# Optimization experiments

Hardware: AMD Instinct MI355X
Metric: run time of the kernel (lower is better)

Reference implementation:

```python
import math
import jax, jax.numpy as jnp
import numpy as np

B, S, D, H, P, FF = 64, 100, 768, 8, 8, 3072
HD = D // H
NUM_LAYERS = 4
EPS = 1e-5


def _layernorm(x, g, b):
    m = jnp.mean(x, axis=-1, keepdims=True)
    v = jnp.mean(jnp.square(x - m), axis=-1, keepdims=True)
    return (x - m) * jax.lax.rsqrt(v + EPS) * g + b


def _positional_encoding(seq_len, d_model):
    pos = jnp.arange(seq_len, dtype=jnp.float32)[:, None]
    div = jnp.exp(jnp.arange(0, d_model, 2, dtype=jnp.float32) * (-math.log(10000.0) / d_model))
    pe = jnp.zeros((seq_len, d_model), dtype=jnp.float32)
    pe = pe.at[:, 0::2].set(jnp.sin(pos * div))
    pe = pe.at[:, 1::2].set(jnp.cos(pos * div))
    return pe[None]  # [1, S, D]


def setup_inputs() -> dict:
    key = jax.random.key(0)
    ks = jax.random.split(key, 12)
    s = 0.02
    return {
        "template_seq": jax.random.normal(ks[0], (B, S, D), jnp.float32),
        "param_seq": jax.random.normal(ks[1], (B, S, P, 768), jnp.float32),
        # ParamEncoder (shared across all 4 layers)
        "Wc": jax.random.normal(ks[2], (768, D), jnp.float32) * s,
        "bc": jnp.zeros((D,), jnp.float32),
        "gp": jnp.ones((D,), jnp.float32),
        "bp": jnp.zeros((D,), jnp.float32),
        # FFN (shared)
        "W1": jax.random.normal(ks[3], (D, FF), jnp.float32) * s,
        "b1": jnp.zeros((FF,), jnp.float32),
        "W2": jax.random.normal(ks[4], (FF, D), jnp.float32) * s,
        "b2": jnp.zeros((D,), jnp.float32),
        # LayerNorms (shared)
        "g1": jnp.ones((D,), jnp.float32),
        "bn1": jnp.zeros((D,), jnp.float32),
        "g2": jnp.ones((D,), jnp.float32),
        "bn2": jnp.zeros((D,), jnp.float32),
        # final classifier
        "Wfc": jax.random.normal(ks[5], (D * S, 2), jnp.float32) * s,
        "bfc": jnp.zeros((2,), jnp.float32),
    }


def _layer(src, param_seq, Wc, bc, gp, bp, W1, b1, W2, b2, g1, bn1, g2, bn2):
    inv_sqrt_hd = 1.0 / math.sqrt(HD)
    # ParamEncoder: Linear(768->D) per param vector, mean over params, LayerNorm.
    # Linear is linear => mean-then-project is identical to project-then-mean.
    pooled = jnp.mean(param_seq, axis=2)                  # [B, S, 768]
    param_enc = _layernorm(pooled @ Wc + bc, gp, bp)       # [B, S, D]
    pb = param_enc.reshape(B, S, H, HD).transpose(0, 2, 1, 3)  # [B, H, S, HD]
    param_bias = jnp.einsum('bhqd,bhkd->bhqk', pb, pb) * inv_sqrt_hd
    # attention with q = k = v = src (no projections in the original forward)
    q = src.reshape(B, S, H, HD).transpose(0, 2, 1, 3)     # [B, H, S, HD]
    attn = jnp.einsum('bhqd,bhkd->bhqk', q, q) * inv_sqrt_hd + param_bias
    attn = jax.nn.softmax(attn, axis=-1)
    out = jnp.einsum('bhqk,bhkd->bhqd', attn, q)
    out = out.transpose(0, 2, 1, 3).reshape(B, S, D)
    src = _layernorm(src + out, g1, bn1)
    ffn = jax.nn.gelu(src @ W1 + b1, approximate=False) @ W2 + b2
    return _layernorm(src + ffn, g2, bn2)


def reference(template_seq, param_seq, Wc, bc, gp, bp, W1, b1, W2, b2,
              g1, bn1, g2, bn2, Wfc, bfc):
    x = template_seq + _positional_encoding(S, D)
    for _ in range(NUM_LAYERS):
        x = _layer(x, param_seq, Wc, bc, gp, bp, W1, b1, W2, b2, g1, bn1, g2, bn2)
    return x.reshape(B, S * D) @ Wfc + bfc  # [B, 2]
```

## Files before the change

kernel.cpp:

```cpp
#include <hip/hip_runtime.h>
#include <hip/hip_bf16.h>
#include <math.h>


typedef __attribute__((ext_vector_type(8))) short bf16x8;
typedef __attribute__((ext_vector_type(4))) float f32x4;
typedef __attribute__((ext_vector_type(4))) short short4v;

#define BB 64
#define SS 100
#define DD 768
#define HH 8
#define HD 96
#define FF_ 3072
#define ROWS 6400
#define LN10000 9.210340371976184f

__device__ __forceinline__ void async_copy16(void* lds_dst, const void* gsrc) {
  __builtin_amdgcn_global_load_lds(
      (const __attribute__((address_space(1))) void*)gsrc,
      (__attribute__((address_space(3))) void*)lds_dst, 16, 0, 0);
}

__device__ __forceinline__ float block_sum256(float v, float* sbuf) {
#pragma unroll
  for (int o = 32; o > 0; o >>= 1) v += __shfl_xor(v, o, 64);
  int tid = threadIdx.x;
  __syncthreads();
  if ((tid & 63) == 0) sbuf[tid >> 6] = v;
  __syncthreads();
  return sbuf[0] + sbuf[1] + sbuf[2] + sbuf[3];
}

__device__ __forceinline__ float block_sum192(float v, float* sbuf) {
#pragma unroll
  for (int o = 32; o > 0; o >>= 1) v += __shfl_xor(v, o, 64);
  int tid = threadIdx.x;
  __syncthreads();
  if ((tid & 63) == 0) sbuf[tid >> 6] = v;
  __syncthreads();
  return sbuf[0] + sbuf[1] + sbuf[2];
}

__global__ void convert_transpose(const float* __restrict__ in,
                                  __hip_bfloat16* __restrict__ out,
                                  int K, int N) {
  __shared__ float t[32][33];
  int n0 = blockIdx.x * 32, k0 = blockIdx.y * 32;
  int tid = threadIdx.x;
  int tx = tid & 31, ty = tid >> 5;
#pragma unroll
  for (int j = 0; j < 32; j += 8)
    t[ty + j][tx] = in[(size_t)(k0 + ty + j) * N + n0 + tx];
  __syncthreads();
#pragma unroll
  for (int j = 0; j < 32; j += 8)
    out[(size_t)(n0 + ty + j) * K + k0 + tx] = __float2bfloat16(t[tx][ty + j]);
}

__global__ void pool_mean(const float* __restrict__ ps,
                          __hip_bfloat16* __restrict__ pooled) {
  int idx = blockIdx.x * 256 + threadIdx.x;
  int row = idx / DD, c = idx - row * DD;
  float s = 0.f;
#pragma unroll
  for (int p = 0; p < 8; p++) s += ps[(size_t)(row * 8 + p) * DD + c];
  pooled[idx] = __float2bfloat16(s * 0.125f);
}

__global__ void add_pe(const float* __restrict__ t, float* __restrict__ src) {
  int idx = blockIdx.x * 256 + threadIdx.x;
  int row = idx / DD, c = idx - row * DD;
  int srow = row % SS;
  int c2 = c & ~1;
  float ang = (float)srow * expf((float)c2 * (-LN10000 / (float)DD));
  float pe = (c & 1) ? cosf(ang) : sinf(ang);
  src[idx] = t[idx] + pe;
}

template <bool XB16, bool RESID, bool WB16>
__global__ void ln_row(const float* __restrict__ Xf,
                       const __hip_bfloat16* __restrict__ Xb,
                       const float* __restrict__ R,
                       const float* __restrict__ g, const float* __restrict__ bb,
                       float* __restrict__ of, __hip_bfloat16* __restrict__ ob) {
  int row = blockIdx.x, tid = threadIdx.x;
  size_t base = (size_t)row * DD;
  int c4 = tid * 4;
  float4 v;
  if constexpr (XB16) {
    short4v xv = *(const short4v*)(Xb + base + c4);
    __hip_bfloat16* p = (__hip_bfloat16*)&xv;
    v.x = __bfloat162float(p[0]); v.y = __bfloat162float(p[1]);
    v.z = __bfloat162float(p[2]); v.w = __bfloat162float(p[3]);
  } else {
    v = *(const float4*)(Xf + base + c4);
  }
  if (RESID) {
    float4 rv = *(const float4*)(R + base + c4);
    v.x += rv.x; v.y += rv.y; v.z += rv.z; v.w += rv.w;
  }
  __shared__ float sbuf[3];
  float s = block_sum192(v.x + v.y + v.z + v.w, sbuf);
  float mean = s * (1.0f / DD);
  float dx = v.x - mean, dy = v.y - mean, dz = v.z - mean, dw = v.w - mean;
  float ss = block_sum192(dx * dx + dy * dy + dz * dz + dw * dw, sbuf);
  float rs = rsqrtf(ss * (1.0f / DD) + 1e-5f);
  float4 gv = *(const float4*)(g + c4);
  float4 bv = *(const float4*)(bb + c4);
  float4 y;
  y.x = dx * rs * gv.x + bv.x;
  y.y = dy * rs * gv.y + bv.y;
  y.z = dz * rs * gv.z + bv.z;
  y.w = dw * rs * gv.w + bv.w;
  *(float4*)(of + base + c4) = y;
  if (WB16) {
    __hip_bfloat16 hb[4] = {__float2bfloat16(y.x), __float2bfloat16(y.y),
                            __float2bfloat16(y.z), __float2bfloat16(y.w)};
    *(short4v*)(ob + base + c4) = *(short4v*)hb;
  }
}

__launch_bounds__(256, 2)
__global__ void param_bias_mfma(const float* __restrict__ penc,
                                float* __restrict__ pbias) {
  __shared__ __align__(16) __hip_bfloat16 Qs[128][104];
  const int bh = blockIdx.x;
  const int b = bh >> 3, h = bh & 7;
  const int tid = threadIdx.x;
  const int wave = tid >> 6, lane = tid & 63;
  const int r = lane & 15, quad = lane >> 4;
  const int q8 = quad * 8;
  const int wr = (wave >> 1) * 64, wc = (wave & 1) * 64;
  const float sroot = rsqrtf(9.79795897113f);
  for (int i = tid; i < 128 * HD; i += 256) {
    int s = i / HD, d = i - s * HD;
    float v = (s < SS) ? penc[(size_t)(b * SS + s) * DD + h * HD + d] : 0.f;
    Qs[s][d] = __float2bfloat16(v * sroot);
  }
  __syncthreads();
  f32x4 acc[4][4] = {};
#pragma unroll
  for (int k0 = 0; k0 < HD; k0 += 32) {
    bf16x8 af[4], bfv[4];
#pragma unroll
    for (int mi = 0; mi < 4; mi++)
      af[mi] = *(const bf16x8*)&Qs[wr + mi * 16 + r][k0 + q8];
#pragma unroll
    for (int ni = 0; ni < 4; ni++)
      bfv[ni] = *(const bf16x8*)&Qs[wc + ni * 16 + r][k0 + q8];
#pragma unroll
    for (int mi = 0; mi < 4; mi++)
#pragma unroll
      for (int ni = 0; ni < 4; ni++)
        acc[mi][ni] = __builtin_amdgcn_mfma_f32_16x16x32_bf16(af[mi], bfv[ni],
                                                              acc[mi][ni], 0, 0, 0);
  }
  float* pb = pbias + (size_t)bh * SS * SS;
#pragma unroll
  for (int mi = 0; mi < 4; mi++)
#pragma unroll
    for (int ni = 0; ni < 4; ni++) {
      int col = wc + ni * 16 + r;
      if (col < SS) {
#pragma unroll
        for (int rg = 0; rg < 4; rg++) {
          int row = wr + mi * 16 + quad * 4 + rg;
          if (row < SS) pb[row * SS + col] = acc[mi][ni][rg];
        }
      }
    }
}

__launch_bounds__(256, 2)
__global__ void attn_fused_mfma(const float* __restrict__ src,
                                const float* __restrict__ pbias,
                                __hip_bfloat16* __restrict__ out) {
  __shared__ __align__(16) char umem[128 * 136 * 2];
  __shared__ __align__(16) __hip_bfloat16 Qt[96][136];
  __shared__ float redm[2][128];
  __shared__ float reds[2][128];
  __hip_bfloat16 (*Qs)[104] = (__hip_bfloat16 (*)[104])umem;
  __hip_bfloat16 (*Ps)[136] = (__hip_bfloat16 (*)[136])umem;

  const int bh = blockIdx.x;
  const int b = bh >> 3, h = bh & 7;
  const int tid = threadIdx.x;
  const int wave = tid >> 6, lane = tid & 63;
  const int r = lane & 15, quad = lane >> 4;
  const int q8 = quad * 8;
  const int wr = (wave >> 1) * 64, wc = (wave & 1) * 64;

  const float sroot = rsqrtf(9.79795897113f);
  for (int i = tid; i < SS * HD; i += 256) {
    int s = i / HD, d = i - s * HD;
    float v = src[(size_t)(b * SS + s) * DD + h * HD + d];
    Qs[s][d] = __float2bfloat16(v * sroot);
    Qt[d][s] = __float2bfloat16(v);
  }
  for (int i = tid; i < 28 * HD; i += 256) {
    int s = i / HD, d = i - s * HD;
    Qs[100 + s][d] = __float2bfloat16(0.f);
    Qt[d][100 + s] = __float2bfloat16(0.f);
  }

  const float* pb = pbias + (size_t)bh * SS * SS;
  bool cv[4]; int cols[4];
#pragma unroll
  for (int ni = 0; ni < 4; ni++) { cols[ni] = wc + ni * 16 + r; cv[ni] = cols[ni] < SS; }
  f32x4 acc[4][4];
#pragma unroll
  for (int mi = 0; mi < 4; mi++)
#pragma unroll
    for (int rg = 0; rg < 4; rg++) {
      int row = wr + mi * 16 + quad * 4 + rg;
#pragma unroll
      for (int ni = 0; ni < 4; ni++)
        acc[mi][ni][rg] = (row < SS && cv[ni]) ? pb[row * SS + cols[ni]] : 0.f;
    }
  __syncthreads();

#pragma unroll
  for (int k0 = 0; k0 < HD; k0 += 32) {
    bf16x8 af[4], bfv[4];
#pragma unroll
    for (int mi = 0; mi < 4; mi++)
      af[mi] = *(const bf16x8*)&Qs[wr + mi * 16 + r][k0 + q8];
#pragma unroll
    for (int ni = 0; ni < 4; ni++)
      bfv[ni] = *(const bf16x8*)&Qs[wc + ni * 16 + r][k0 + q8];
#pragma unroll
    for (int mi = 0; mi < 4; mi++)
#pragma unroll
      for (int ni = 0; ni < 4; ni++)
        acc[mi][ni] = __builtin_amdgcn_mfma_f32_16x16x32_bf16(af[mi], bfv[ni],
                                                              acc[mi][ni], 0, 0, 0);
  }

  float mx[4][4];
#pragma unroll
  for (int mi = 0; mi < 4; mi++)
#pragma unroll
    for (int rg = 0; rg < 4; rg++) {
      float m = -1e30f;
#pragma unroll
      for (int ni = 0; ni < 4; ni++)
        if (cv[ni]) m = fmaxf(m, acc[mi][ni][rg]);
#pragma unroll
      for (int o = 1; o < 16; o <<= 1) m = fmaxf(m, __shfl_xor(m, o, 64));
      mx[mi][rg] = m;
    }
  if (r == 0) {
#pragma unroll
    for (int mi = 0; mi < 4; mi++)
#pragma unroll
      for (int rg = 0; rg < 4; rg++)
        redm[wave & 1][wr + mi * 16 + quad * 4 + rg] = mx[mi][rg];
  }
  __syncthreads();

#pragma unroll
  for (int mi = 0; mi < 4; mi++)
#pragma unroll
    for (int rg = 0; rg < 4; rg++) {
      int row = wr + mi * 16 + quad * 4 + rg;
      float rmax = fmaxf(redm[0][row], redm[1][row]);
      float s = 0.f;
#pragma unroll
      for (int ni = 0; ni < 4; ni++) {
        float e = cv[ni] ? __expf(acc[mi][ni][rg] - rmax) : 0.f;
        acc[mi][ni][rg] = e;
        s += e;
      }
#pragma unroll
      for (int o = 1; o < 16; o <<= 1) s += __shfl_xor(s, o, 64);
      if (r == 0) reds[wave & 1][row] = s;
    }
  __syncthreads();

#pragma unroll
  for (int mi = 0; mi < 4; mi++)
#pragma unroll
    for (int rg = 0; rg < 4; rg++) {
      int row = wr + mi * 16 + quad * 4 + rg;
      float inv = 1.0f / (reds[0][row] + reds[1][row]);
#pragma unroll
      for (int ni = 0; ni < 4; ni++)
        Ps[row][cols[ni]] = __float2bfloat16(acc[mi][ni][rg] * inv);
    }
  __syncthreads();

  const int wr2 = (wave >> 1) * 48;
  f32x4 po[3][4] = {};
#pragma unroll
  for (int kk = 0; kk < 128; kk += 32) {
    bf16x8 aq[3], bp[4];
#pragma unroll
    for (int mi = 0; mi < 3; mi++)
      aq[mi] = *(const bf16x8*)&Qt[wr2 + mi * 16 + r][kk + q8];
#pragma unroll
    for (int ni = 0; ni < 4; ni++)
      bp[ni] = *(const bf16x8*)&Ps[wc + ni * 16 + r][kk + q8];
#pragma unroll
    for (int mi = 0; mi < 3; mi++)
#pragma unroll
      for (int ni = 0; ni < 4; ni++)
        po[mi][ni] = __builtin_amdgcn_mfma_f32_16x16x32_bf16(aq[mi], bp[ni],
                                                             po[mi][ni], 0, 0, 0);
  }
#pragma unroll
  for (int mi = 0; mi < 3; mi++)
#pragma unroll
    for (int ni = 0; ni < 4; ni++) {
      int qcol = wc + ni * 16 + r;
      if (qcol < SS) {
        int d0 = wr2 + mi * 16 + quad * 4;
        __hip_bfloat16 hb[4];
#pragma unroll
        for (int rg = 0; rg < 4; rg++) hb[rg] = __float2bfloat16(po[mi][ni][rg]);
        *(short4v*)(out + (size_t)(b * SS + qcol) * DD + h * HD + d0) = *(short4v*)hb;
      }
    }
}

template <int MODE>
__launch_bounds__(256)
__global__ void gemm_bt(const __hip_bfloat16* __restrict__ A,
                        const __hip_bfloat16* __restrict__ Bt,
                        const float* __restrict__ bias,
                        const float* __restrict__ resid,
                        float* __restrict__ outf,
                        __hip_bfloat16* __restrict__ outb,
                        int M, int N, int K) {
  constexpr int BM = 128, BN = 128, BK = 32;
  __shared__ __align__(16) __hip_bfloat16 As[2][BM * BK];
  __shared__ __align__(16) __hip_bfloat16 Bs[2][BN * BK];
  const int tid = threadIdx.x;
  const int wave = tid >> 6, lane = tid & 63;
  const int wr = (wave >> 1) * 64, wc = (wave & 1) * 64;
  const int m0 = blockIdx.y * BM, n0 = blockIdx.x * BN;
  const int r = lane & 15, q = lane >> 4;
  const int q8 = q * 8;
  const int key8 = ((r >> 1) & 3) * 8;

  const int liA = tid, liB = tid + 256;
  const int rowA = liA >> 2, rowB = liB >> 2;
  const int cpA = (liA & 3) ^ ((rowA >> 1) & 3);
  const int cpB = (liB & 3) ^ ((rowB >> 1) & 3);
  const __hip_bfloat16* gA0 = A + (size_t)(m0 + rowA) * K + cpA * 8;
  const __hip_bfloat16* gA1 = A + (size_t)(m0 + rowB) * K + cpB * 8;
  const __hip_bfloat16* gB0 = Bt + (size_t)(n0 + rowA) * K + cpA * 8;
  const __hip_bfloat16* gB1 = Bt + (size_t)(n0 + rowB) * K + cpB * 8;

  f32x4 acc[4][4] = {};

  auto stage = [&](int buf, int k0) {
    async_copy16(&As[buf][liA * 8], gA0 + k0);
    async_copy16(&As[buf][liB * 8], gA1 + k0);
    async_copy16(&Bs[buf][liA * 8], gB0 + k0);
    async_copy16(&Bs[buf][liB * 8], gB1 + k0);
  };
  auto compute = [&](int buf) {
    bf16x8 af[4], bfr[4];
#pragma unroll
    for (int mi = 0; mi < 4; mi++)
      af[mi] = *(const bf16x8*)(&As[buf][(wr + mi * 16 + r) * BK + (q8 ^ key8)]);
#pragma unroll
    for (int ni = 0; ni < 4; ni++)
      bfr[ni] = *(const bf16x8*)(&Bs[buf][(wc + ni * 16 + r) * BK + (q8 ^ key8)]);
#pragma unroll
    for (int mi = 0; mi < 4; mi++)
#pragma unroll
      for (int ni = 0; ni < 4; ni++)
        acc[mi][ni] = __builtin_amdgcn_mfma_f32_16x16x32_bf16(af[mi], bfr[ni],
                                                              acc[mi][ni], 0, 0, 0);
  };

  const int NT = K / BK;
  stage(0, 0);
  __syncthreads();
  int cur = 0;
  for (int t = 0; t < NT - 1; ++t) {
    stage(cur ^ 1, (t + 1) * BK);
    compute(cur);
    __syncthreads();
    cur ^= 1;
  }
  compute(cur);

#pragma unroll
  for (int mi = 0; mi < 4; mi++) {
#pragma unroll
    for (int ni = 0; ni < 4; ni++) {
      int col = n0 + wc + ni * 16 + r;
      float bv = bias[col];
#pragma unroll
      for (int rg = 0; rg < 4; rg++) {
        int row = m0 + wr + mi * 16 + q * 4 + rg;
        size_t oidx = (size_t)row * N + col;
        float v = acc[mi][ni][rg] + bv;
        if constexpr (MODE == 2) v += resid[oidx];
        if constexpr (MODE == 1) {
          v = 0.5f * v * (1.0f + erff(v * 0.70710678118654752f));
          outb[oidx] = __float2bfloat16(v);
        } else {
          outf[oidx] = v;
        }
      }
    }
  }
}

#define CCHUNK 3072
#define NCHUNK 25
__global__ void classifier_part(const float* __restrict__ x,
                                const float* __restrict__ Wfc,
                                float* __restrict__ part) {
  int chunk = blockIdx.x, b = blockIdx.y, tid = threadIdx.x;
  const float* xb = x + (size_t)b * (SS * DD) + chunk * CCHUNK;
  const float* w = Wfc + 2 * (size_t)chunk * CCHUNK;
  float a0 = 0.f, a1 = 0.f;
  for (int i = tid; i < CCHUNK; i += 256) {
    float xv = xb[i];
    float2 wv = *(const float2*)(w + 2 * i);
    a0 += xv * wv.x;
    a1 += xv * wv.y;
  }
  __shared__ float sbuf[4];
  a0 = block_sum256(a0, sbuf);
  a1 = block_sum256(a1, sbuf);
  if (tid == 0) {
    part[(b * NCHUNK + chunk) * 2] = a0;
    part[(b * NCHUNK + chunk) * 2 + 1] = a1;
  }
}

__global__ void classifier_final(const float* __restrict__ part,
                                 const float* __restrict__ bfc,
                                 float* __restrict__ out) {
  int b = threadIdx.x;
  float a0 = bfc[0], a1 = bfc[1];
#pragma unroll
  for (int c = 0; c < NCHUNK; c++) {
    a0 += part[(b * NCHUNK + c) * 2];
    a1 += part[(b * NCHUNK + c) * 2 + 1];
  }
  out[2 * b] = a0;
  out[2 * b + 1] = a1;
}

extern "C" void kernel_launch(void* const* d_in, const int* in_sizes, int n_in,
                              void* d_out, int out_size, void* d_ws, size_t ws_size,
                              hipStream_t stream) {
  const float* Tmpl = (const float*)d_in[0];
  const float* Pseq = (const float*)d_in[1];
  const float* Wc   = (const float*)d_in[2];
  const float* bc   = (const float*)d_in[3];
  const float* gp   = (const float*)d_in[4];
  const float* bp   = (const float*)d_in[5];
  const float* W1   = (const float*)d_in[6];
  const float* b1   = (const float*)d_in[7];
  const float* W2   = (const float*)d_in[8];
  const float* b2   = (const float*)d_in[9];
  const float* g1   = (const float*)d_in[10];
  const float* bn1  = (const float*)d_in[11];
  const float* g2   = (const float*)d_in[12];
  const float* bn2  = (const float*)d_in[13];
  const float* Wfc  = (const float*)d_in[14];
  const float* bfc  = (const float*)d_in[15];
  float* out = (float*)d_out;
  (void)in_sizes; (void)n_in; (void)out_size; (void)ws_size;

  char* ws = (char*)d_ws;
  size_t off = 0;
  auto alloc = [&](size_t n) { size_t o = off; off += (n + 255) & ~(size_t)255; return o; };

  __hip_bfloat16* Wct = (__hip_bfloat16*)(ws + alloc((size_t)768 * 768 * 2));
  __hip_bfloat16* W1t = (__hip_bfloat16*)(ws + alloc((size_t)768 * 3072 * 2));
  __hip_bfloat16* W2t = (__hip_bfloat16*)(ws + alloc((size_t)3072 * 768 * 2));
  size_t h1_off = alloc((size_t)ROWS * FF_ * 2);
  __hip_bfloat16* h1 = (__hip_bfloat16*)(ws + h1_off);
  float* param_enc = (float*)(ws + h1_off);
  size_t slb_off = alloc((size_t)ROWS * DD * 2);
  __hip_bfloat16* src_ln_bf = (__hip_bfloat16*)(ws + slb_off);
  __hip_bfloat16* pooled = (__hip_bfloat16*)(ws + slb_off);
  size_t ao_off = alloc((size_t)ROWS * DD * 4);
  __hip_bfloat16* attn_out_b = (__hip_bfloat16*)(ws + ao_off);
  float* pe_lin = (float*)(ws + ao_off);
  float* pbias = (float*)(ws + alloc((size_t)512 * SS * SS * 4));
  float* src = (float*)(ws + alloc((size_t)ROWS * DD * 4));
  float* src_ln = (float*)(ws + alloc((size_t)ROWS * DD * 4));
  float* z = (float*)(ws + alloc((size_t)ROWS * DD * 4));
  float* cpart = (float*)(ws + alloc((size_t)BB * NCHUNK * 2 * 4));

  convert_transpose<<<dim3(768 / 32, 768 / 32), 256, 0, stream>>>(Wc, Wct, 768, 768);
  convert_transpose<<<dim3(3072 / 32, 768 / 32), 256, 0, stream>>>(W1, W1t, 768, 3072);
  convert_transpose<<<dim3(768 / 32, 3072 / 32), 256, 0, stream>>>(W2, W2t, 3072, 768);
  pool_mean<<<ROWS * DD / 256, 256, 0, stream>>>(Pseq, pooled);
  gemm_bt<0><<<dim3(DD / 128, ROWS / 128), 256, 0, stream>>>(
      pooled, Wct, bc, nullptr, pe_lin, nullptr, ROWS, DD, 768);
  ln_row<false, false, false><<<ROWS, 192, 0, stream>>>(
      pe_lin, nullptr, nullptr, gp, bp, param_enc, nullptr);
  param_bias_mfma<<<512, 256, 0, stream>>>(param_enc, pbias);
  add_pe<<<ROWS * DD / 256, 256, 0, stream>>>(Tmpl, src);

  for (int l = 0; l < 4; ++l) {
    attn_fused_mfma<<<512, 256, 0, stream>>>(src, pbias, attn_out_b);
    ln_row<true, true, true><<<ROWS, 192, 0, stream>>>(
        nullptr, attn_out_b, src, g1, bn1, src_ln, src_ln_bf);
    gemm_bt<1><<<dim3(FF_ / 128, ROWS / 128), 256, 0, stream>>>(
        src_ln_bf, W1t, b1, nullptr, nullptr, h1, ROWS, FF_, DD);
    gemm_bt<2><<<dim3(DD / 128, ROWS / 128), 256, 0, stream>>>(
        h1, W2t, b2, src_ln, z, nullptr, ROWS, DD, FF_);
    ln_row<false, false, false><<<ROWS, 192, 0, stream>>>(
        z, nullptr, nullptr, g2, bn2, src, nullptr);
  }

  classifier_part<<<dim3(NCHUNK, BB), 256, 0, stream>>>(src, Wfc, cpart);
  classifier_final<<<1, 64, 0, stream>>>(cpart, bfc, out);
}
```

Baseline: 1.075 ms.

## Enlarge GEMM tile to 256x128 with 512 threads and triple-buffered async loads

The bf16 MFMA GEMM now uses a 256x128 block tile with 8 waves and 512 threads. Its LDS double buffer becomes a three-stage ring. Loads for tile t+2 are issued after computing tile t, and explicit vmcnt waits plus raw barriers replace the single syncthreads per step, so global-to-LDS copies overlap more with MFMA work and each B tile is reused across more rows. The trade-off is that the grid for the N=768 GEMMs halves to 150 blocks, fewer than the CU count, and LDS use per block rises to about 72KB.

```diff
diff --git a/kernel.cpp b/kernel.cpp
--- a/kernel.cpp
+++ b/kernel.cpp
@@ -324,7 +324,7 @@
 }
 
 template <int MODE>
-__launch_bounds__(256)
+__launch_bounds__(512)
 __global__ void gemm_bt(const __hip_bfloat16* __restrict__ A,
                         const __hip_bfloat16* __restrict__ Bt,
                         const float* __restrict__ bias,
@@ -332,9 +332,9 @@
                         float* __restrict__ outf,
                         __hip_bfloat16* __restrict__ outb,
                         int M, int N, int K) {
-  constexpr int BM = 128, BN = 128, BK = 32;
-  __shared__ __align__(16) __hip_bfloat16 As[2][BM * BK];
-  __shared__ __align__(16) __hip_bfloat16 Bs[2][BN * BK];
+  constexpr int BM = 256, BN = 128, BK = 32;
+  __shared__ __align__(16) __hip_bfloat16 As[3][BM * BK];
+  __shared__ __align__(16) __hip_bfloat16 Bs[3][BN * BK];
   const int tid = threadIdx.x;
   const int wave = tid >> 6, lane = tid & 63;
   const int wr = (wave >> 1) * 64, wc = (wave & 1) * 64;
@@ -343,22 +343,19 @@
   const int q8 = q * 8;
   const int key8 = ((r >> 1) & 3) * 8;
 
-  const int liA = tid, liB = tid + 256;
-  const int rowA = liA >> 2, rowB = liB >> 2;
-  const int cpA = (liA & 3) ^ ((rowA >> 1) & 3);
-  const int cpB = (liB & 3) ^ ((rowB >> 1) & 3);
-  const __hip_bfloat16* gA0 = A + (size_t)(m0 + rowA) * K + cpA * 8;
-  const __hip_bfloat16* gA1 = A + (size_t)(m0 + rowB) * K + cpB * 8;
-  const __hip_bfloat16* gB0 = Bt + (size_t)(n0 + rowA) * K + cpA * 8;
-  const __hip_bfloat16* gB1 = Bt + (size_t)(n0 + rowB) * K + cpB * 8;
+  const int rowA0 = tid >> 2;
+  const int cp0 = (tid & 3) ^ ((rowA0 >> 1) & 3);
+  const int rowA1 = rowA0 + 128;
+  const __hip_bfloat16* gA0 = A + (size_t)(m0 + rowA0) * K + cp0 * 8;
+  const __hip_bfloat16* gA1 = A + (size_t)(m0 + rowA1) * K + cp0 * 8;
+  const __hip_bfloat16* gB0 = Bt + (size_t)(n0 + rowA0) * K + cp0 * 8;
 
   f32x4 acc[4][4] = {};
 
   auto stage = [&](int buf, int k0) {
-    async_copy16(&As[buf][liA * 8], gA0 + k0);
-    async_copy16(&As[buf][liB * 8], gA1 + k0);
-    async_copy16(&Bs[buf][liA * 8], gB0 + k0);
-    async_copy16(&Bs[buf][liB * 8], gB1 + k0);
+    async_copy16(&As[buf][tid * 8], gA0 + k0);
+    async_copy16(&As[buf][(tid + 512) * 8], gA1 + k0);
+    async_copy16(&Bs[buf][tid * 8], gB0 + k0);
   };
   auto compute = [&](int buf) {
     bf16x8 af[4], bfr[4];
@@ -378,15 +375,21 @@
 
   const int NT = K / BK;
   stage(0, 0);
-  __syncthreads();
-  int cur = 0;
-  for (int t = 0; t < NT - 1; ++t) {
-    stage(cur ^ 1, (t + 1) * BK);
-    compute(cur);
-    __syncthreads();
-    cur ^= 1;
-  }
-  compute(cur);
+  stage(1, BK);
+  int cb = 0, sb = 2;
+  for (int t = 0; t < NT; ++t) {
+    if (t < NT - 1) {
+      asm volatile("s_waitcnt vmcnt(3)" ::: "memory");
+    } else {
+      asm volatile("s_waitcnt vmcnt(0)" ::: "memory");
+    }
+    __builtin_amdgcn_s_barrier();
+    compute(cb);
+    __builtin_amdgcn_s_barrier();
+    if (t + 2 < NT) stage(sb, (t + 2) * BK);
+    cb = (cb == 2) ? 0 : cb + 1;
+    sb = (sb == 2) ? 0 : sb + 1;
+  }
 
 #pragma unroll
   for (int mi = 0; mi < 4; mi++) {
@@ -497,7 +500,7 @@
   convert_transpose<<<dim3(3072 / 32, 768 / 32), 256, 0, stream>>>(W1, W1t, 768, 3072);
   convert_transpose<<<dim3(768 / 32, 3072 / 32), 256, 0, stream>>>(W2, W2t, 3072, 768);
   pool_mean<<<ROWS * DD / 256, 256, 0, stream>>>(Pseq, pooled);
-  gemm_bt<0><<<dim3(DD / 128, ROWS / 128), 256, 0, stream>>>(
+  gemm_bt<0><<<dim3(DD / 128, ROWS / 256), 512, 0, stream>>>(
       pooled, Wct, bc, nullptr, pe_lin, nullptr, ROWS, DD, 768);
   ln_row<false, false, false><<<ROWS, 192, 0, stream>>>(
       pe_lin, nullptr, nullptr, gp, bp, param_enc, nullptr);
@@ -508,9 +511,9 @@
     attn_fused_mfma<<<512, 256, 0, stream>>>(src, pbias, attn_out_b);
     ln_row<true, true, true><<<ROWS, 192, 0, stream>>>(
         nullptr, attn_out_b, src, g1, bn1, src_ln, src_ln_bf);
-    gemm_bt<1><<<dim3(FF_ / 128, ROWS / 128), 256, 0, stream>>>(
+    gemm_bt<1><<<dim3(FF_ / 128, ROWS / 256), 512, 0, stream>>>(
         src_ln_bf, W1t, b1, nullptr, nullptr, h1, ROWS, FF_, DD);
-    gemm_bt<2><<<dim3(DD / 128, ROWS / 128), 256, 0, stream>>>(
+    gemm_bt<2><<<dim3(DD / 128, ROWS / 256), 512, 0, stream>>>(
         h1, W2t, b2, src_ln, z, nullptr, ROWS, DD, FF_);
     ln_row<false, false, false><<<ROWS, 192, 0, stream>>>(
         z, nullptr, nullptr, g2, bn2, src, nullptr);
```

New measurement: 1.058 ms. About the same (-1.6%).
